# Kernel tuning notes

Hardware: AMD Instinct MI355X
Metric: run time of the kernel (lower is better)

The kernel has to match this reference:

```python
import jax, jax.numpy as jnp
import numpy as np
from jax import lax

EPS = 1e-5
NUM_HEADS = 8


def _safe_norm(x):
    # sqrt(max(sum x^2, EPS^2)) == max(||x||, EPS); grad-safe at 0
    return jnp.sqrt(jnp.maximum(jnp.sum(x * x, axis=-1, keepdims=True), EPS * EPS))


def _project(x):
    norm = _safe_norm(x)
    max_norm = 1.0 - EPS
    scale = jnp.where(norm >= max_norm, max_norm / (norm + EPS), jnp.ones_like(norm))
    return x * scale


def _logmap0(y):
    # logarithmic_map(0, y): lambda_0 = 2/(1+EPS)
    y = _project(y)
    n = _safe_norm(y)  # clamp(min=EPS) is built in
    lam = 2.0 / (1.0 + EPS)
    return (2.0 / lam) * jnp.arctanh(n) * (y / n)


def _expmap0(v):
    # exponential_map(0, v): lambda_0 = 2/(1+EPS)
    n = _safe_norm(v)
    lam = 2.0 / (1.0 + EPS)
    return _project(jnp.tanh(lam * n / 2.0) * (v / n))


def _mobius_add(x, y):
    x = _project(x)
    y = _project(y)
    xy = jnp.sum(x * y, axis=-1, keepdims=True)
    xn = jnp.sum(x * x, axis=-1, keepdims=True)
    yn = jnp.sum(y * y, axis=-1, keepdims=True)
    num = (1.0 + 2.0 * xy + yn) * x + (1.0 - xn) * y
    den = 1.0 + 2.0 * xy + xn * yn + EPS
    return _project(num / den)


def _hyp_linear(x, W, b):
    # HyperbolicLinear.forward: project -> logmap0 -> linear -> expmap0 -> mobius-add bias
    x = _project(x)
    xt = _logmap0(x)
    t = xt @ W.T
    r = _expmap0(t)
    r = _mobius_add(r, jnp.broadcast_to(b, r.shape))
    return r


def setup_inputs() -> dict:
    key = jax.random.key(0)
    ks = jax.random.split(key, 11)
    B, S, E = 4, 512, 512

    def xavier(k, shape):
        bound = np.sqrt(6.0 / (shape[0] + shape[1]))
        return jax.random.uniform(k, shape, jnp.float32, -bound, bound)

    return {
        "query": jax.random.normal(ks[0], (B, S, E), jnp.float32),
        "key": jax.random.normal(ks[1], (B, S, E), jnp.float32),
        "value": jax.random.normal(ks[2], (B, S, E), jnp.float32),
        "Wq": xavier(ks[3], (E, E)), "bq": 0.01 * jax.random.normal(ks[4], (E,), jnp.float32),
        "Wk": xavier(ks[5], (E, E)), "bk": 0.01 * jax.random.normal(ks[6], (E,), jnp.float32),
        "Wv": xavier(ks[7], (E, E)), "bv": 0.01 * jax.random.normal(ks[8], (E,), jnp.float32),
        "Wo": xavier(ks[9], (E, E)), "bo": 0.01 * jax.random.normal(ks[10], (E,), jnp.float32),
    }


def reference(query, key, value, Wq, bq, Wk, bk, Wv, bv, Wo, bo):
    B, S, E = query.shape
    H = NUM_HEADS
    D = E // H

    Q = _hyp_linear(query, Wq, bq).reshape(B, S, H, D).transpose(0, 2, 1, 3)  # [B,H,S,D]
    K = _hyp_linear(key, Wk, bk).reshape(B, S, H, D).transpose(0, 2, 1, 3)
    V = _hyp_linear(value, Wv, bv).reshape(B, S, H, D).transpose(0, 2, 1, 3)

    # Pairwise Poincare distance: d(q,k) = acosh(1 + 2||q-k||^2/((1-|q|^2)(1-|k|^2)) + EPS)
    q = _project(Q)
    k = _project(K)
    qn = jnp.sum(q * q, axis=-1)  # [B,H,S]
    kn = jnp.sum(k * k, axis=-1)  # [B,H,S]
    qk = jnp.einsum('bhqd,bhkd->bhqk', q, k)
    num = jnp.maximum(qn[..., :, None] + kn[..., None, :] - 2.0 * qk, 0.0)
    den = jnp.maximum((1.0 - qn)[..., :, None] * (1.0 - kn)[..., None, :], EPS)
    dist = jnp.arccosh(1.0 + 2.0 * num / den + EPS)  # [B,H,Sq,Sk]
    attn = jax.nn.softmax(-dist, axis=-1)

    # Sequential Mobius-add accumulation over key/value positions
    wt = jnp.moveaxis(attn, 3, 0)  # [Sk,B,H,Sq]
    vt = jnp.moveaxis(V, 2, 0)     # [Sk,B,H,D]

    @jax.checkpoint
    def step(ws, wv):
        wj, vj = wv  # wj: [B,H,Sq], vj: [B,H,D]
        return _mobius_add(ws, wj[..., None] * vj[:, :, None, :]), None

    ws0 = jnp.zeros((B, H, S, D), query.dtype)
    attended, _ = lax.scan(step, ws0, (wt, vt))  # [B,H,Sq,D]

    attended = attended.transpose(0, 2, 1, 3).reshape(B, S, E)
    return _hyp_linear(attended, Wo, bo)
```

## Files before the change

kernel.cpp:

```cpp
#include <hip/hip_runtime.h>
#include <math.h>

#define EPS  1e-5f
#define EPS2 1e-10f
#define MAXN (1.0f - EPS)

using short8  = __attribute__((ext_vector_type(8))) short;
using floatx4 = __attribute__((ext_vector_type(4))) float;

template <int CTRL>
static __device__ __forceinline__ float qperm(float x) {
  return __int_as_float(__builtin_amdgcn_update_dpp(
      __float_as_int(x), __float_as_int(x), CTRL, 0xF, 0xF, false));
}
#define QP_XOR1    0xB1
#define QP_XOR2    0x4E
#define QP_HALFMIR 0x141

static __device__ __forceinline__ short bf16_rne(float x) {
  unsigned u = __float_as_uint(x);
  unsigned r = u + 0x7FFFu + ((u >> 16) & 1u);
  return (short)(r >> 16);
}
static __device__ __forceinline__ float bf16_tof(short h) {
  return __uint_as_float(((unsigned)(unsigned short)h) << 16);
}

static __device__ __forceinline__ float logmap_f(float ss) {
  const float r = sqrtf(fmaxf(ss, EPS2));
  float at;
  if (r >= MAXN) {
    at = 0.5f * logf((r * (2.0f - EPS) + EPS) / (EPS * (1.0f + r)));
  } else {
    at = 0.5f * logf((1.0f + r) / (1.0f - r));
  }
  return (1.0f + EPS) * at / r;
}

__global__ __launch_bounds__(256) void k_gemm_mfma(
    const float* __restrict__ A0, const float* __restrict__ A1, const float* __restrict__ A2,
    const float* __restrict__ W0, const float* __restrict__ W1, const float* __restrict__ W2,
    float* __restrict__ Cbase) {
  const int z = blockIdx.z;
  const float* A = (z == 0) ? A0 : ((z == 1) ? A1 : A2);
  const float* W = (z == 0) ? W0 : ((z == 1) ? W1 : W2);
  float* C = Cbase + (size_t)z * (2048 * 512);
  __shared__ short Ahi[64][72], Alo[64][72], Whi[64][72], Wlo[64][72];
  __shared__ float f_lds[64];
  const int t = threadIdx.x;
  const int n0 = blockIdx.x * 64;
  const int m0 = blockIdx.y * 64;
  const int row = t >> 2, c0 = (t & 3) * 16;
  const int w = t >> 6, lane = t & 63;
  const int quad = lane >> 4, l16 = lane & 15;
  const int mw = (w & 1) * 32, nw = (w >> 1) * 32;
  floatx4 acc[2][2];
#pragma unroll
  for (int i = 0; i < 2; ++i)
#pragma unroll
    for (int j = 0; j < 2; ++j) acc[i][j] = (floatx4){0.f, 0.f, 0.f, 0.f};
  float ssq = 0.0f;

  for (int k0 = 0; k0 < 512; k0 += 64) {
    float4 av[4], wv[4];
#pragma unroll
    for (int i = 0; i < 4; ++i) {
      av[i] = *(const float4*)&A[(size_t)(n0 + row) * 512 + k0 + c0 + 4 * i];
      wv[i] = *(const float4*)&W[(size_t)(m0 + row) * 512 + k0 + c0 + 4 * i];
    }
    __syncthreads();
#pragma unroll
    for (int i = 0; i < 4; ++i) {
      const float a4[4] = {av[i].x, av[i].y, av[i].z, av[i].w};
      const float w4[4] = {wv[i].x, wv[i].y, wv[i].z, wv[i].w};
#pragma unroll
      for (int e = 0; e < 4; ++e) {
        ssq = fmaf(a4[e], a4[e], ssq);
        const short ah = bf16_rne(a4[e]);
        const short wh = bf16_rne(w4[e]);
        Ahi[row][c0 + 4 * i + e] = ah;
        Alo[row][c0 + 4 * i + e] = bf16_rne(a4[e] - bf16_tof(ah));
        Whi[row][c0 + 4 * i + e] = wh;
        Wlo[row][c0 + 4 * i + e] = bf16_rne(w4[e] - bf16_tof(wh));
      }
    }
    __syncthreads();
#pragma unroll
    for (int kk = 0; kk < 64; kk += 32) {
      short8 ah[2], al[2], bh[2], bl[2];
#pragma unroll
      for (int i = 0; i < 2; ++i) {
        ah[i] = *(const short8*)&Ahi[mw + i * 16 + l16][kk + quad * 8];
        al[i] = *(const short8*)&Alo[mw + i * 16 + l16][kk + quad * 8];
        bh[i] = *(const short8*)&Whi[nw + i * 16 + l16][kk + quad * 8];
        bl[i] = *(const short8*)&Wlo[nw + i * 16 + l16][kk + quad * 8];
      }
#pragma unroll
      for (int i = 0; i < 2; ++i)
#pragma unroll
        for (int j = 0; j < 2; ++j) {
          acc[i][j] = __builtin_amdgcn_mfma_f32_16x16x32_bf16(ah[i], bh[j], acc[i][j], 0, 0, 0);
          acc[i][j] = __builtin_amdgcn_mfma_f32_16x16x32_bf16(ah[i], bl[j], acc[i][j], 0, 0, 0);
          acc[i][j] = __builtin_amdgcn_mfma_f32_16x16x32_bf16(al[i], bh[j], acc[i][j], 0, 0, 0);
        }
    }
  }
  ssq += qperm<QP_XOR1>(ssq);
  ssq += qperm<QP_XOR2>(ssq);
  if ((t & 3) == 0) f_lds[row] = logmap_f(ssq);
  __syncthreads();
#pragma unroll
  for (int i = 0; i < 2; ++i) {
    const int lrow_base = mw + i * 16 + quad * 4;
#pragma unroll
    for (int r = 0; r < 4; ++r) {
      const float fv = f_lds[lrow_base + r];
#pragma unroll
      for (int j = 0; j < 2; ++j)
        C[(size_t)(n0 + lrow_base + r) * 512 + m0 + nw + j * 16 + l16] = fv * acc[i][j][r];
    }
  }
}

__global__ __launch_bounds__(256) void k_post(const float* __restrict__ tin,
                                              const float* __restrict__ b0,
                                              const float* __restrict__ b1,
                                              const float* __restrict__ b2,
                                              float* __restrict__ o0, float* __restrict__ o1,
                                              float* __restrict__ o2,
                                              float* __restrict__ nrm0, float* __restrict__ nrm1,
                                              float* __restrict__ nrm2,
                                              float* __restrict__ rowsum_init, int final_mode) {
  const int nrow = blockIdx.x, z = blockIdx.y, t = threadIdx.x;
  const float* tv = tin + ((size_t)z * 2048 + nrow) * 512;
  const float* bias = (z == 0) ? b0 : ((z == 1) ? b1 : b2);
  const int e0 = 2 * t;
  const float2 tp = *(const float2*)&tv[e0];
  const float2 bp = *(const float2*)&bias[e0];
  float p_tt = tp.x * tp.x + tp.y * tp.y;
  float p_tb = tp.x * bp.x + tp.y * bp.y;
  float p_bb = bp.x * bp.x + bp.y * bp.y;
#pragma unroll
  for (int m = 32; m; m >>= 1) {
    p_tt += __shfl_xor(p_tt, m, 64);
    p_tb += __shfl_xor(p_tb, m, 64);
    p_bb += __shfl_xor(p_bb, m, 64);
  }
  __shared__ float red[4][3];
  const int lane = t & 63, w = t >> 6;
  if (lane == 0) { red[w][0] = p_tt; red[w][1] = p_tb; red[w][2] = p_bb; }
  __syncthreads();
  const float s_tt = red[0][0] + red[1][0] + red[2][0] + red[3][0];
  const float s_tb = red[0][1] + red[1][1] + red[2][1] + red[3][1];
  const float s_bb = red[0][2] + red[1][2] + red[2][2] + red[3][2];
  const float tn = sqrtf(fmaxf(s_tt, EPS2));
  const float th = tanhf(tn / (1.0f + EPS));
  const float g = th / tn;
  const float rnorm = th * (sqrtf(s_tt) / tn);
  const float sr = (rnorm >= MAXN) ? (MAXN / (rnorm + EPS)) : 1.0f;
  const float gr = g * sr;
  const float rn = (rnorm * sr) * (rnorm * sr);
  const float bnorm = sqrtf(fmaxf(s_bb, EPS2));
  const float sb = (bnorm >= MAXN) ? (MAXN / (bnorm + EPS)) : 1.0f;
  const float xy = gr * sb * s_tb;
  const float yn = (sb * sb) * s_bb;
  const float Af = 1.0f + 2.0f * xy + yn;
  const float Cf = 1.0f - rn;
  const float den = 1.0f + 2.0f * xy + rn * yn + EPS;
  const float id = 1.0f / den;
  const float on_raw = (Af * Af * rn + 2.0f * Af * Cf * xy + Cf * Cf * yn) * (id * id);
  const float no = sqrtf(fmaxf(on_raw, EPS2));
  const float so = (no >= MAXN) ? (MAXN / (no + EPS)) : 1.0f;
  const float ms = id * so;
  const float ca = gr * Af * ms;
  const float cb = sb * Cf * ms;
  const float v0 = ca * tp.x + cb * bp.x;
  const float v1 = ca * tp.y + cb * bp.y;
  if (final_mode) {
    float2 o; o.x = v0; o.y = v1;
    *(float2*)&o0[(size_t)nrow * 512 + e0] = o;
    return;
  }
  float hp = v0 * v0 + v1 * v1;
#pragma unroll
  for (int m = 16; m; m >>= 1) hp += __shfl_xor(hp, m, 64);
  const float hnr = sqrtf(fmaxf(hp, EPS2));
  float sh = 1.0f;
  if (z != 2) sh = (hnr >= MAXN) ? (MAXN / (hnr + EPS)) : 1.0f;
  float* outz = (z == 0) ? o0 : ((z == 1) ? o1 : o2);
  float* nz = (z == 0) ? nrm0 : ((z == 1) ? nrm1 : nrm2);
  const int b = nrow >> 9, s = nrow & 511, h = e0 >> 6, d = e0 & 63;
  float2 o; o.x = v0 * sh; o.y = v1 * sh;
  *(float2*)&outz[(((size_t)(b * 8 + h) * 512 + s) * 64 + d)] = o;
  if ((t & 31) == 0) nz[(size_t)(b * 8 + h) * 512 + s] = hp * sh * sh;
  if (z == 0 && t < 8) rowsum_init[((size_t)(nrow >> 9) * 8 + t) * 512 + (nrow & 511)] = 0.0f;
}

__global__ __launch_bounds__(256) void k_logits(const float* __restrict__ Q,
                                                const float* __restrict__ K,
                                                const float* __restrict__ qn,
                                                const float* __restrict__ kn,
                                                float* __restrict__ attn,
                                                float* __restrict__ rowsum) {
  const int bh = blockIdx.z;
  const int i0 = blockIdx.x * 64;
  const int j0 = blockIdx.y * 128;
  const float* Qb = Q + (size_t)bh * 512 * 64;
  const float* Kb = K + (size_t)bh * 512 * 64;
  __shared__ __align__(16) float q_lds[64][68];
  __shared__ __align__(16) float k_lds[128][68];
  const int t = threadIdx.x;
  const int tx = t & 15, ty = t >> 4;
  const int tx4 = tx * 4;
#pragma unroll
  for (int it = 0; it < 4; ++it) {
    const int row = it * 16 + ty;
    *(float4*)&q_lds[row][tx4] = *(const float4*)&Qb[(size_t)(i0 + row) * 64 + tx4];
  }
#pragma unroll
  for (int it = 0; it < 8; ++it) {
    const int row = it * 16 + ty;
    *(float4*)&k_lds[row][tx4] = *(const float4*)&Kb[(size_t)(j0 + row) * 64 + tx4];
  }
  __syncthreads();
  float acc[4][8] = {};
#pragma unroll
  for (int d = 0; d < 64; d += 4) {
    float4 qv[4], kv[8];
#pragma unroll
    for (int i = 0; i < 4; ++i) qv[i] = *(const float4*)&q_lds[ty * 4 + i][d];
#pragma unroll
    for (int j = 0; j < 8; ++j) kv[j] = *(const float4*)&k_lds[tx + 16 * j][d];
#pragma unroll
    for (int i = 0; i < 4; ++i)
#pragma unroll
      for (int j = 0; j < 8; ++j) {
        acc[i][j] = fmaf(qv[i].x, kv[j].x, acc[i][j]);
        acc[i][j] = fmaf(qv[i].y, kv[j].y, acc[i][j]);
        acc[i][j] = fmaf(qv[i].z, kv[j].z, acc[i][j]);
        acc[i][j] = fmaf(qv[i].w, kv[j].w, acc[i][j]);
      }
  }
  float qni[4], knj[8];
#pragma unroll
  for (int i = 0; i < 4; ++i) qni[i] = qn[(size_t)bh * 512 + i0 + ty * 4 + i];
#pragma unroll
  for (int j = 0; j < 8; ++j) knj[j] = kn[(size_t)bh * 512 + j0 + tx + 16 * j];
  float rs_[4] = {};
#pragma unroll
  for (int i = 0; i < 4; ++i)
#pragma unroll
    for (int j = 0; j < 8; ++j) {
      const float num = fmaxf(qni[i] + knj[j] - 2.0f * acc[i][j], 0.0f);
      const float den = fmaxf((1.0f - qni[i]) * (1.0f - knj[j]), EPS);
      const float wv = 2.0f * num / den + EPS;
      const float s_ = 1.0f + wv + sqrtf(wv * (wv + 2.0f));
      const float r = __builtin_amdgcn_rcpf(s_);
      rs_[i] += r;
      attn[((size_t)bh * 512 + i0 + ty * 4 + i) * 512 + j0 + tx + 16 * j] = r;
    }
#pragma unroll
  for (int i = 0; i < 4; ++i) {
    float v = rs_[i];
    v += __shfl_xor(v, 1, 64); v += __shfl_xor(v, 2, 64);
    v += __shfl_xor(v, 4, 64); v += __shfl_xor(v, 8, 64);
    if (tx == 0) atomicAdd(&rowsum[(size_t)bh * 512 + i0 + ty * 4 + i], v);
  }
}

__global__ __launch_bounds__(256) void k_scan(const float* __restrict__ V,
                                              const float* __restrict__ vn,
                                              const float* __restrict__ rw,
                                              const float* __restrict__ rowsum,
                                              float* __restrict__ att) {
  __shared__ __align__(16) float v_lds[64 * 64];
  __shared__ __align__(16) float swyn_lds[64 * 66];
  const int blk = blockIdx.x;
  const int bh = blk >> 4;
  const int i0 = (blk & 15) * 32;
  const int t = threadIdx.x;
  const int lane = t & 63, w = t >> 6;
  const int row_blk = w * 8 + (lane >> 3);
  const int sub = lane & 7;
  const int d0 = sub * 8;
  const float* Vb = V + (size_t)bh * 512 * 64;
  const float* vnb = vn + (size_t)bh * 512;
  const float* arow = rw + ((size_t)bh * 512 + i0 + row_blk) * 512;
  const float inv_s = __builtin_amdgcn_rcpf(rowsum[(size_t)bh * 512 + i0 + row_blk]);

  float ws[8];
#pragma unroll
  for (int k = 0; k < 8; ++k) ws[k] = 0.0f;
  float xn = 0.0f;

  for (int jc = 0; jc < 512; jc += 64) {
#pragma unroll
    for (int it = 0; it < 4; ++it) {
      const int idx4 = it * 256 + t;
      *(float4*)&v_lds[idx4 * 4] = *(const float4*)&Vb[(size_t)jc * 64 + idx4 * 4];
    }
    const float4 a0 = *(const float4*)&arow[jc + sub * 8];
    const float4 a1 = *(const float4*)&arow[jc + sub * 8 + 4];
    const float4 n0 = *(const float4*)&vnb[jc + sub * 8];
    const float4 n1 = *(const float4*)&vnb[jc + sub * 8 + 4];
    const float wq[8] = {a0.x, a0.y, a0.z, a0.w, a1.x, a1.y, a1.z, a1.w};
    const float nq[8] = {n0.x, n0.y, n0.z, n0.w, n1.x, n1.y, n1.z, n1.w};
#pragma unroll
    for (int e = 0; e < 8; ++e) {
      const float wgt = wq[e] * inv_s;
      float2 p; p.x = wgt; p.y = (wgt * wgt) * nq[e];
      *(float2*)&swyn_lds[(sub * 8 + e) * 66 + row_blk * 2] = p;
    }
    __syncthreads();

#pragma unroll 16
    for (int j = 0; j < 64; ++j) {
      const float2 sy2 = *(const float2*)&swyn_lds[j * 66 + row_blk * 2];
      const float4 v0 = *(const float4*)&v_lds[j * 64 + d0];
      const float4 v1 = *(const float4*)&v_lds[j * 64 + d0 + 4];
      const float sw = sy2.x, yn = sy2.y;
      const float xnyn1 = fmaf(xn, yn, 1.0f + EPS);
      const float sxy   = xn + yn;
      const float ynp1  = 1.0f + yn;
      const float Cfsw  = (1.0f - xn) * sw;
      float da = ws[0] * v0.x;
      da = fmaf(ws[1], v0.y, da); da = fmaf(ws[2], v0.z, da); da = fmaf(ws[3], v0.w, da);
      float db = ws[4] * v1.x;
      db = fmaf(ws[5], v1.y, db); db = fmaf(ws[6], v1.z, db); db = fmaf(ws[7], v1.w, db);
      float d = da + db;
      d += qperm<QP_XOR1>(d);
      d += qperm<QP_XOR2>(d);
      d += qperm<QP_HALFMIR>(d);
      const float xy  = sw * d;
      const float den = fmaf(2.0f, xy, xnyn1);
      const float s2  = fmaf(2.0f, xy, sxy);
      const float Af  = fmaf(2.0f, xy, ynp1);
      const float id  = __builtin_amdgcn_rcpf(den);
      const float dn  = den - EPS;
      const float am  = Af * id;
      const float cm  = Cfsw * id;
      const float xa  = s2 * id;
      const float xb  = dn * id;
      xn = xa * xb;
      ws[0] = fmaf(am, ws[0], cm * v0.x); ws[1] = fmaf(am, ws[1], cm * v0.y);
      ws[2] = fmaf(am, ws[2], cm * v0.z); ws[3] = fmaf(am, ws[3], cm * v0.w);
      ws[4] = fmaf(am, ws[4], cm * v1.x); ws[5] = fmaf(am, ws[5], cm * v1.y);
      ws[6] = fmaf(am, ws[6], cm * v1.z); ws[7] = fmaf(am, ws[7], cm * v1.w);
    }
    __syncthreads();
  }
  const int b = bh >> 3, h = bh & 7;
  float* o = att + (((size_t)b * 512 + i0 + row_blk) * 512 + h * 64 + d0);
  float4 s0; s0.x = ws[0]; s0.y = ws[1]; s0.z = ws[2]; s0.w = ws[3];
  float4 s1; s1.x = ws[4]; s1.y = ws[5]; s1.z = ws[6]; s1.w = ws[7];
  *(float4*)&o[0] = s0;
  *(float4*)&o[4] = s1;
}

extern "C" void kernel_launch(void* const* d_in, const int* in_sizes, int n_in,
                              void* d_out, int out_size, void* d_ws, size_t ws_size,
                              hipStream_t stream) {
  const float* query = (const float*)d_in[0];
  const float* key_  = (const float*)d_in[1];
  const float* value = (const float*)d_in[2];
  const float* Wq = (const float*)d_in[3];
  const float* bq = (const float*)d_in[4];
  const float* Wk = (const float*)d_in[5];
  const float* bk = (const float*)d_in[6];
  const float* Wv = (const float*)d_in[7];
  const float* bv = (const float*)d_in[8];
  const float* Wo = (const float*)d_in[9];
  const float* bo = (const float*)d_in[10];
  float* ws = (float*)d_ws;
  const size_t M = 1u << 20;
  float* Qb     = ws;
  float* Kb     = ws + 1 * M;
  float* Vb     = ws + 2 * M;
  float* qn     = ws + 3 * M;
  float* kn     = qn + 16384;
  float* vn     = kn + 16384;
  float* rowsum = vn + 16384;
  float* rw     = ws + 4 * M;
  float* t3     = ws + 12 * M;
  float* att    = ws + 15 * M;
  float* to_    = ws + 16 * M;

  k_gemm_mfma<<<dim3(32, 8, 3), 256, 0, stream>>>(query, key_, value, Wq, Wk, Wv, t3);
  k_post<<<dim3(2048, 3), 256, 0, stream>>>(t3, bq, bk, bv, Qb, Kb, Vb, qn, kn, vn,
                                            rowsum, 0);
  k_logits<<<dim3(8, 4, 32), 256, 0, stream>>>(Qb, Kb, qn, kn, rw, rowsum);
  k_scan<<<512, 256, 0, stream>>>(Vb, vn, rw, rowsum, att);
  k_gemm_mfma<<<dim3(32, 8, 1), 256, 0, stream>>>(att, att, att, Wo, Wo, Wo, to_);
  k_post<<<dim3(2048, 1), 256, 0, stream>>>(to_, bo, bo, bo, (float*)d_out,
                                            nullptr, nullptr, nullptr, nullptr, nullptr,
                                            nullptr, 1);
}
```

Baseline: 279.4 us.

## Compute logits QK^T with split-bf16 MFMA and fully unroll scan loop

Rewrites the pairwise-distance logits kernel to use bf16 MFMA instructions, splitting each fp32 operand into high and low bf16 parts and doing three MFMAs to approximate fp32 accuracy. Tile shape drops to 64x64 per block, so the grid doubles. The division in the distance is replaced by a hardware reciprocal. The scan's inner loop over 64 keys is fully unrolled. Split-bf16 products lose some precision compared with fp32 FMA, which can shift the acosh distances near zero, and full unrolling raises register pressure.

```diff
diff --git a/kernel.cpp b/kernel.cpp
--- a/kernel.cpp
+++ b/kernel.cpp
@@ -204,67 +204,89 @@
                                                 float* __restrict__ rowsum) {
   const int bh = blockIdx.z;
   const int i0 = blockIdx.x * 64;
-  const int j0 = blockIdx.y * 128;
+  const int j0 = blockIdx.y * 64;
   const float* Qb = Q + (size_t)bh * 512 * 64;
   const float* Kb = K + (size_t)bh * 512 * 64;
-  __shared__ __align__(16) float q_lds[64][68];
-  __shared__ __align__(16) float k_lds[128][68];
+  __shared__ short Qhi[64][72], Qlo[64][72], Khi[64][72], Klo[64][72];
   const int t = threadIdx.x;
-  const int tx = t & 15, ty = t >> 4;
-  const int tx4 = tx * 4;
-#pragma unroll
-  for (int it = 0; it < 4; ++it) {
-    const int row = it * 16 + ty;
-    *(float4*)&q_lds[row][tx4] = *(const float4*)&Qb[(size_t)(i0 + row) * 64 + tx4];
-  }
-#pragma unroll
-  for (int it = 0; it < 8; ++it) {
-    const int row = it * 16 + ty;
-    *(float4*)&k_lds[row][tx4] = *(const float4*)&Kb[(size_t)(j0 + row) * 64 + tx4];
+  const int row = t >> 2, c0 = (t & 3) * 16;
+  const int w = t >> 6, lane = t & 63;
+  const int quad = lane >> 4, l16 = lane & 15;
+  const int mw = (w & 1) * 32, nw = (w >> 1) * 32;
+  float4 qv4[4], kv4[4];
+#pragma unroll
+  for (int i = 0; i < 4; ++i) {
+    qv4[i] = *(const float4*)&Qb[(size_t)(i0 + row) * 64 + c0 + 4 * i];
+    kv4[i] = *(const float4*)&Kb[(size_t)(j0 + row) * 64 + c0 + 4 * i];
+  }
+#pragma unroll
+  for (int i = 0; i < 4; ++i) {
+    const float q4[4] = {qv4[i].x, qv4[i].y, qv4[i].z, qv4[i].w};
+    const float k4[4] = {kv4[i].x, kv4[i].y, kv4[i].z, kv4[i].w};
+#pragma unroll
+    for (int e = 0; e < 4; ++e) {
+      const short qh = bf16_rne(q4[e]);
+      const short kh = bf16_rne(k4[e]);
+      Qhi[row][c0 + 4 * i + e] = qh;
+      Qlo[row][c0 + 4 * i + e] = bf16_rne(q4[e] - bf16_tof(qh));
+      Khi[row][c0 + 4 * i + e] = kh;
+      Klo[row][c0 + 4 * i + e] = bf16_rne(k4[e] - bf16_tof(kh));
+    }
   }
   __syncthreads();
-  float acc[4][8] = {};
-#pragma unroll
-  for (int d = 0; d < 64; d += 4) {
-    float4 qv[4], kv[8];
-#pragma unroll
-    for (int i = 0; i < 4; ++i) qv[i] = *(const float4*)&q_lds[ty * 4 + i][d];
-#pragma unroll
-    for (int j = 0; j < 8; ++j) kv[j] = *(const float4*)&k_lds[tx + 16 * j][d];
-#pragma unroll
-    for (int i = 0; i < 4; ++i)
-#pragma unroll
-      for (int j = 0; j < 8; ++j) {
-        acc[i][j] = fmaf(qv[i].x, kv[j].x, acc[i][j]);
-        acc[i][j] = fmaf(qv[i].y, kv[j].y, acc[i][j]);
-        acc[i][j] = fmaf(qv[i].z, kv[j].z, acc[i][j]);
-        acc[i][j] = fmaf(qv[i].w, kv[j].w, acc[i][j]);
+  floatx4 acc[2][2];
+#pragma unroll
+  for (int i = 0; i < 2; ++i)
+#pragma unroll
+    for (int j = 0; j < 2; ++j) acc[i][j] = (floatx4){0.f, 0.f, 0.f, 0.f};
+#pragma unroll
+  for (int kk = 0; kk < 64; kk += 32) {
+    short8 ah[2], al[2], bhv[2], blv[2];
+#pragma unroll
+    for (int i = 0; i < 2; ++i) {
+      ah[i] = *(const short8*)&Qhi[mw + i * 16 + l16][kk + quad * 8];
+      al[i] = *(const short8*)&Qlo[mw + i * 16 + l16][kk + quad * 8];
+      bhv[i] = *(const short8*)&Khi[nw + i * 16 + l16][kk + quad * 8];
+      blv[i] = *(const short8*)&Klo[nw + i * 16 + l16][kk + quad * 8];
+    }
+#pragma unroll
+    for (int i = 0; i < 2; ++i)
+#pragma unroll
+      for (int j = 0; j < 2; ++j) {
+        acc[i][j] = __builtin_amdgcn_mfma_f32_16x16x32_bf16(ah[i], bhv[j], acc[i][j], 0, 0, 0);
+        acc[i][j] = __builtin_amdgcn_mfma_f32_16x16x32_bf16(ah[i], blv[j], acc[i][j], 0, 0, 0);
+        acc[i][j] = __builtin_amdgcn_mfma_f32_16x16x32_bf16(al[i], bhv[j], acc[i][j], 0, 0, 0);
       }
   }
-  float qni[4], knj[8];
-#pragma unroll
-  for (int i = 0; i < 4; ++i) qni[i] = qn[(size_t)bh * 512 + i0 + ty * 4 + i];
-#pragma unroll
-  for (int j = 0; j < 8; ++j) knj[j] = kn[(size_t)bh * 512 + j0 + tx + 16 * j];
-  float rs_[4] = {};
-#pragma unroll
-  for (int i = 0; i < 4; ++i)
-#pragma unroll
-    for (int j = 0; j < 8; ++j) {
-      const float num = fmaxf(qni[i] + knj[j] - 2.0f * acc[i][j], 0.0f);
-      const float den = fmaxf((1.0f - qni[i]) * (1.0f - knj[j]), EPS);
-      const float wv = 2.0f * num / den + EPS;
-      const float s_ = 1.0f + wv + sqrtf(wv * (wv + 2.0f));
-      const float r = __builtin_amdgcn_rcpf(s_);
-      rs_[i] += r;
-      attn[((size_t)bh * 512 + i0 + ty * 4 + i) * 512 + j0 + tx + 16 * j] = r;
-    }
-#pragma unroll
-  for (int i = 0; i < 4; ++i) {
-    float v = rs_[i];
-    v += __shfl_xor(v, 1, 64); v += __shfl_xor(v, 2, 64);
-    v += __shfl_xor(v, 4, 64); v += __shfl_xor(v, 8, 64);
-    if (tx == 0) atomicAdd(&rowsum[(size_t)bh * 512 + i0 + ty * 4 + i], v);
+#pragma unroll
+  for (int i = 0; i < 2; ++i) {
+    float rs_acc[4] = {0.f, 0.f, 0.f, 0.f};
+#pragma unroll
+    for (int r = 0; r < 4; ++r) {
+      const int grow = i0 + mw + i * 16 + quad * 4 + r;
+      const float qni = qn[(size_t)bh * 512 + grow];
+      const float rq = 1.0f - qni;
+#pragma unroll
+      for (int j = 0; j < 2; ++j) {
+        const int gcol = j0 + nw + j * 16 + l16;
+        const float knj = kn[(size_t)bh * 512 + gcol];
+        const float num = fmaxf(qni + knj - 2.0f * acc[i][j][r], 0.0f);
+        const float den = fmaxf(rq * (1.0f - knj), EPS);
+        const float wv = fmaf(2.0f * num, __builtin_amdgcn_rcpf(den), EPS);
+        const float s_ = 1.0f + wv + sqrtf(wv * (wv + 2.0f));
+        const float rr = __builtin_amdgcn_rcpf(s_);
+        rs_acc[r] += rr;
+        attn[((size_t)bh * 512 + grow) * 512 + gcol] = rr;
+      }
+    }
+#pragma unroll
+    for (int r = 0; r < 4; ++r) {
+      float v = rs_acc[r];
+      v += __shfl_xor(v, 1, 64); v += __shfl_xor(v, 2, 64);
+      v += __shfl_xor(v, 4, 64); v += __shfl_xor(v, 8, 64);
+      if (l16 == 0)
+        atomicAdd(&rowsum[(size_t)bh * 512 + i0 + mw + i * 16 + quad * 4 + r], v);
+    }
   }
 }
 
@@ -313,7 +335,7 @@
     }
     __syncthreads();
 
-#pragma unroll 16
+#pragma unroll
     for (int j = 0; j < 64; ++j) {
       const float2 sy2 = *(const float2*)&swyn_lds[j * 66 + row_blk * 2];
       const float4 v0 = *(const float4*)&v_lds[j * 64 + d0];
@@ -388,7 +410,7 @@
   k_gemm_mfma<<<dim3(32, 8, 3), 256, 0, stream>>>(query, key_, value, Wq, Wk, Wv, t3);
   k_post<<<dim3(2048, 3), 256, 0, stream>>>(t3, bq, bk, bv, Qb, Kb, Vb, qn, kn, vn,
                                             rowsum, 0);
-  k_logits<<<dim3(8, 4, 32), 256, 0, stream>>>(Qb, Kb, qn, kn, rw, rowsum);
+  k_logits<<<dim3(8, 8, 32), 256, 0, stream>>>(Qb, Kb, qn, kn, rw, rowsum);
   k_scan<<<512, 256, 0, stream>>>(Vb, vn, rw, rowsum, att);
   k_gemm_mfma<<<dim3(32, 8, 1), 256, 0, stream>>>(att, att, att, Wo, Wo, Wo, to_);
   k_post<<<dim3(2048, 1), 256, 0, stream>>>(to_, bo, bo, bo, (float*)d_out,
```

Result: faster. 255.5 us (-8.6%).
